# Kernel optimization log

Hardware: AMD Instinct MI355X
Metric: run time of the kernel (lower is better)

The kernel has to match this reference:

```python
import jax, jax.numpy as jnp
import numpy as np

B, D, H = 4096, 256, 1024
TRACE_STEPS = 10
T_FINAL = 1.0


def setup_inputs() -> dict:
    key = jax.random.key(0)
    k0, k1, k2 = jax.random.split(key, 3)
    s1 = 1.0 / np.sqrt(D + 1)
    s2 = 1.0 / np.sqrt(H)
    return {
        "x": jax.random.normal(k0, (B, D), dtype=jnp.float32),
        "W1": jax.random.uniform(k1, (D + 1, H), jnp.float32, -s1, s1),
        "b1": jnp.zeros((H,), jnp.float32),
        "W2": jax.random.uniform(k2, (H, D), jnp.float32, -s2, s2),
        "b2": jnp.zeros((D,), jnp.float32),
    }


def _odefun(params, t, z):
    # FFJORD vector field: tanh MLP on [z, t]. z: [B, D] -> [B, D]
    W1, b1, W2, b2 = params
    tcol = jnp.full((z.shape[0], 1), t, dtype=z.dtype)
    h = jnp.tanh(jnp.concatenate([z, tcol], axis=-1) @ W1 + b1)
    return h @ W2 + b2


def _rademacher(key, shape, dtype):
    # randint(0,2)*2-1, matching the torch probe construction
    return jax.random.randint(key, shape, 0, 2).astype(dtype) * 2.0 - 1.0


def _aug_dynamics(params, t, state, e):
    # state: [B, D+1] = [z | logp]; e: [TRACE_STEPS, B, D] Rademacher probes.
    # torch computes etf = grad((f*e).sum(), z) = e^T J, div = (e^T J)*e summed.
    # e^T J e == e . (J e), so forward-mode jvp gives identical math.
    z = state[:, :-1]
    f = lambda zz: _odefun(params, t, zz)

    def probe(ei):
        f_z, Je = jax.jvp(f, (z,), (ei,))
        return f_z, jnp.sum(Je * ei, axis=-1)  # [B]

    f_z, divs = jax.vmap(probe)(e)
    f_z = f_z[0]                       # primal identical across probes
    div_est = jnp.mean(divs, axis=0)   # average of trace_steps estimates
    return jnp.concatenate([f_z, -div_est[:, None]], axis=-1)


def reference(x, W1, b1, W2, b2):
    params = (W1, b1, W2, b2)
    Bx = x.shape[0]
    ekey = jax.random.key(42)
    probes = lambda i: _rademacher(jax.random.fold_in(ekey, i), (TRACE_STEPS, Bx, D), x.dtype)

    # initial augmented state: [z, logp=0]
    y0 = jnp.concatenate([x, jnp.zeros((Bx, 1), x.dtype)], axis=-1)

    # t_grid = [0, T] with 2 points -> fixed-grid rk4 takes ONE RK4 step of size T
    h = T_FINAL
    g = lambda t, y, i: _aug_dynamics(params, t, y, probes(i))
    k1 = g(0.0, y0, 0)
    k2 = g(0.5 * h, y0 + 0.5 * h * k1, 1)
    k3 = g(0.5 * h, y0 + 0.5 * h * k2, 2)
    k4 = g(h, y0 + h * k3, 3)
    y1 = y0 + (h / 6.0) * (k1 + 2.0 * k2 + 2.0 * k3 + k4)

    # module returns the full trajectory `output`: [len(t_grid), B, D+1]
    return jnp.stack([y0, y1], axis=0)
```

## Files before the change

### kernel.cpp

```cpp
#include <hip/hip_runtime.h>
#include <stdint.h>

#define BATCH 4096
#define DIMD  256
#define DIMH  1024
#define EPAD  264

typedef __attribute__((ext_vector_type(8))) short short8;
typedef __attribute__((ext_vector_type(4))) float float4v;

__host__ __device__ static inline uint32_t rotl32(uint32_t v, int r) {
    return (v << r) | (v >> (32 - r));
}

__host__ __device__ static inline void tf2x32(uint32_t k0, uint32_t k1,
                                              uint32_t c0, uint32_t c1,
                                              uint32_t& o0, uint32_t& o1) {
    uint32_t ks0 = k0, ks1 = k1, ks2 = k0 ^ k1 ^ 0x1BD11BDAu;
    uint32_t x0 = c0 + ks0, x1 = c1 + ks1;
#define TF_R4(a, b, c, d)                                   \
    x0 += x1; x1 = rotl32(x1, a); x1 ^= x0;                 \
    x0 += x1; x1 = rotl32(x1, b); x1 ^= x0;                 \
    x0 += x1; x1 = rotl32(x1, c); x1 ^= x0;                 \
    x0 += x1; x1 = rotl32(x1, d); x1 ^= x0;
    TF_R4(13, 15, 26, 6)  x0 += ks1; x1 += ks2 + 1u;
    TF_R4(17, 29, 16, 24) x0 += ks2; x1 += ks0 + 2u;
    TF_R4(13, 15, 26, 6)  x0 += ks0; x1 += ks1 + 3u;
    TF_R4(17, 29, 16, 24) x0 += ks1; x1 += ks2 + 4u;
    TF_R4(13, 15, 26, 6)  x0 += ks2; x1 += ks0 + 5u;
#undef TF_R4
    o0 = x0; o1 = x1;
}

__device__ static inline short f2bf(float f) {
    uint32_t u = __float_as_uint(f);
    uint32_t r = (u + 0x7FFFu + ((u >> 16) & 1u)) >> 16;
    return (short)r;
}
__device__ static inline float bf2f(short s) {
    return __uint_as_float(((uint32_t)(uint16_t)s) << 16);
}

__global__ __launch_bounds__(256) void k_w1t_bf16(
    const float* __restrict__ W1, short* __restrict__ W1T)
{
    __shared__ float tile[32][33];
    const int bx = blockIdx.x;
    const int by = blockIdx.y;
    const int tx = threadIdx.x, ty = threadIdx.y;
#pragma unroll
    for (int i = 0; i < 4; ++i)
        tile[ty + i * 8][tx] = W1[(by * 32 + ty + i * 8) * DIMH + bx * 32 + tx];
    __syncthreads();
#pragma unroll
    for (int i = 0; i < 4; ++i)
        W1T[(bx * 32 + ty + i * 8) * DIMD + by * 32 + tx] = f2bf(tile[tx][ty + i * 8]);
}

__global__ __launch_bounds__(256) void k_w2t_bf16(
    const float* __restrict__ W2, short* __restrict__ W2T)
{
    __shared__ float tile[32][33];
    const int bx = blockIdx.x;
    const int by = blockIdx.y;
    const int tx = threadIdx.x, ty = threadIdx.y;
#pragma unroll
    for (int i = 0; i < 4; ++i)
        tile[ty + i * 8][tx] = W2[(bx * 32 + ty + i * 8) * DIMD + by * 32 + tx];
    __syncthreads();
#pragma unroll
    for (int i = 0; i < 4; ++i)
        W2T[(by * 32 + ty + i * 8) * DIMH + bx * 32 + tx] = f2bf(tile[tx][ty + i * 8]);
}

__global__ __launch_bounds__(256) void k_w2b_bf16(
    const float* __restrict__ W2, short* __restrict__ W2B)
{
    int idx = blockIdx.x * 256 + threadIdx.x;
    if (idx < DIMH * DIMD) W2B[idx] = f2bf(W2[idx]);
}
__global__ __launch_bounds__(256) void k_zb0(
    const float* __restrict__ x, short* __restrict__ zb)
{
    int idx = blockIdx.x * 256 + threadIdx.x;
    if (idx < BATCH * DIMD) zb[idx] = f2bf(x[idx]);
}

__global__ __launch_bounds__(256) void k_egen(
    uint64_t* __restrict__ Ep, uint32_t key0, uint32_t key1)
{
    const uint32_t j = blockIdx.x * 256 + threadIdx.x;
    uint32_t y0, y1;
    tf2x32(key0, key1, 0u, j, y0, y1);
    uint64_t mask = __ballot(((y0 ^ y1) & 1u) != 0u);
    if ((threadIdx.x & 63) == 0)
        Ep[j >> 6] = mask;
}

__global__ __launch_bounds__(256) void k_pre(
    const short* __restrict__ Zb, const short* __restrict__ W1T,
    const float* __restrict__ W1, const float* __restrict__ b1, float tval,
    short* __restrict__ h_bf)
{
    const int t = threadIdx.x;
    const int wave = t >> 6, lane = t & 63;
    const int col = lane & 15, kq = lane >> 4;
    const int m0 = blockIdx.x * 64 + wave * 16;
    const int n0 = blockIdx.y * 128;

    short8 af[8];
#pragma unroll
    for (int ks = 0; ks < 8; ++ks)
        af[ks] = *(const short8*)&Zb[(m0 + col) * DIMD + ks * 32 + kq * 8];

    float4v acc[8];
#pragma unroll
    for (int ns = 0; ns < 8; ++ns) acc[ns] = (float4v){0.f, 0.f, 0.f, 0.f};

#pragma unroll
    for (int ns = 0; ns < 8; ++ns) {
        const int n = n0 + ns * 16 + col;
        const short* bp = &W1T[n * DIMD + kq * 8];
#pragma unroll
        for (int ks = 0; ks < 8; ++ks) {
            short8 bf = *(const short8*)&bp[ks * 32];
            acc[ns] = __builtin_amdgcn_mfma_f32_16x16x32_bf16(af[ks], bf, acc[ns], 0, 0, 0);
        }
    }
#pragma unroll
    for (int ns = 0; ns < 8; ++ns) {
        const int n = n0 + ns * 16 + col;
        const float add = tval * W1[DIMD * DIMH + n] + b1[n];
#pragma unroll
        for (int r = 0; r < 4; ++r) {
            const int m = m0 + kq * 4 + r;
            h_bf[m * DIMH + n] = f2bf(tanhf(acc[ns][r] + add));
        }
    }
}

__global__ __launch_bounds__(256) void k_fz2(
    const short* __restrict__ Hb, const short* __restrict__ W2T,
    const float* __restrict__ b2, const float* __restrict__ x,
    float* __restrict__ fz, float cnext, int write_zb, short* __restrict__ zb)
{
    const int t = threadIdx.x;
    const int wave = t >> 6, lane = t & 63;
    const int col = lane & 15, kq = lane >> 4;
    const int m0 = blockIdx.x * 16;
    const int n0 = wave * 64;

    float4v acc[4];
#pragma unroll
    for (int ns = 0; ns < 4; ++ns) acc[ns] = (float4v){0.f, 0.f, 0.f, 0.f};

    const short* ap = &Hb[(m0 + col) * DIMH + kq * 8];
    short8 a_cur = *(const short8*)ap;
    short8 b_cur[4];
#pragma unroll
    for (int ns = 0; ns < 4; ++ns)
        b_cur[ns] = *(const short8*)&W2T[(n0 + ns * 16 + col) * DIMH + kq * 8];

    for (int ks = 0; ks < 31; ++ks) {
        short8 a_nxt = *(const short8*)&ap[(ks + 1) * 32];
        short8 b_nxt[4];
#pragma unroll
        for (int ns = 0; ns < 4; ++ns)
            b_nxt[ns] = *(const short8*)&W2T[(n0 + ns * 16 + col) * DIMH + (ks + 1) * 32 + kq * 8];
#pragma unroll
        for (int ns = 0; ns < 4; ++ns)
            acc[ns] = __builtin_amdgcn_mfma_f32_16x16x32_bf16(a_cur, b_cur[ns], acc[ns], 0, 0, 0);
        a_cur = a_nxt;
#pragma unroll
        for (int ns = 0; ns < 4; ++ns) b_cur[ns] = b_nxt[ns];
    }
#pragma unroll
    for (int ns = 0; ns < 4; ++ns)
        acc[ns] = __builtin_amdgcn_mfma_f32_16x16x32_bf16(a_cur, b_cur[ns], acc[ns], 0, 0, 0);

#pragma unroll
    for (int ns = 0; ns < 4; ++ns) {
        const int n = n0 + ns * 16 + col;
        const float bias = b2[n];
#pragma unroll
        for (int r = 0; r < 4; ++r) {
            const int m = m0 + kq * 4 + r;
            const float val = acc[ns][r] + bias;
            fz[m * DIMD + n] = val;
            if (write_zb)
                zb[m * DIMD + n] = f2bf(x[m * DIMD + n] + cnext * val);
        }
    }
}

__global__ __launch_bounds__(256) void k_div2(
    const short* __restrict__ W1T, const short* __restrict__ W2B,
    const short* __restrict__ Hb, const uint64_t* __restrict__ Ep,
    float* __restrict__ divacc)
{
    __shared__ short E[64 * EPAD];
    const int t = threadIdx.x;
    const int nt = blockIdx.x;
    const int b0 = blockIdx.y * 64;
    const int wave = t >> 6, lane = t & 63;
    const int col = lane & 15, kq = lane >> 4;
    const int n = nt * 64 + wave * 16 + col;

    short8 bufr[8], bvfr[8];
#pragma unroll
    for (int ks = 0; ks < 8; ++ks) {
        bufr[ks] = *(const short8*)&W1T[n * DIMD + ks * 32 + kq * 8];
        bvfr[ks] = *(const short8*)&W2B[n * DIMD + ks * 32 + kq * 8];
    }

    float sreg[4][4];
#pragma unroll
    for (int ms = 0; ms < 4; ++ms)
#pragma unroll
        for (int r = 0; r < 4; ++r) {
            float hv = bf2f(Hb[(b0 + ms * 16 + kq * 4 + r) * DIMH + n]);
            sreg[ms][r] = 1.0f - hv * hv;
        }

    float rowacc[4][4];
#pragma unroll
    for (int a = 0; a < 4; ++a)
#pragma unroll
        for (int r = 0; r < 4; ++r) rowacc[a][r] = 0.0f;

    const int erow = t >> 2, ecol = (t & 3) * 64;
    short* const edst = &E[erow * EPAD + ecol];

#pragma unroll 1
    for (int probe = 0; probe < 10; ++probe) {
        __syncthreads();
        uint64_t w = Ep[(size_t)(probe * BATCH + b0) * 4 + t];
#pragma unroll
        for (int i = 0; i < 8; ++i) {
            short8 val;
#pragma unroll
            for (int k = 0; k < 8; ++k)
                val[k] = ((w >> (i * 8 + k)) & 1ull) ? (short)0x3F80 : (short)0xBF80u;
            *(short8*)&edst[i * 8] = val;
        }
        __syncthreads();

#pragma unroll
        for (int ms = 0; ms < 4; ++ms) {
            const short* arow = &E[(ms * 16 + col) * EPAD + kq * 8];
            float4v u = {0.f, 0.f, 0.f, 0.f}, v = {0.f, 0.f, 0.f, 0.f};
#pragma unroll
            for (int ks = 0; ks < 8; ++ks) {
                short8 af = *(const short8*)&arow[ks * 32];
                u = __builtin_amdgcn_mfma_f32_16x16x32_bf16(af, bufr[ks], u, 0, 0, 0);
                v = __builtin_amdgcn_mfma_f32_16x16x32_bf16(af, bvfr[ks], v, 0, 0, 0);
            }
#pragma unroll
            for (int r = 0; r < 4; ++r)
                rowacc[ms][r] += u[r] * sreg[ms][r] * v[r];
        }
    }

#pragma unroll
    for (int ms = 0; ms < 4; ++ms) {
#pragma unroll
        for (int r = 0; r < 4; ++r) {
            float p = rowacc[ms][r];
            p += __shfl_xor(p, 1, 64);
            p += __shfl_xor(p, 2, 64);
            p += __shfl_xor(p, 4, 64);
            p += __shfl_xor(p, 8, 64);
            rowacc[ms][r] = p;
        }
    }
    if (col == 0) {
#pragma unroll
        for (int ms = 0; ms < 4; ++ms)
#pragma unroll
            for (int r = 0; r < 4; ++r)
                atomicAdd(&divacc[b0 + ms * 16 + kq * 4 + r], rowacc[ms][r] * 0.1f);
    }
}

__global__ __launch_bounds__(256) void k_out(
    const float* __restrict__ x, const float* __restrict__ fz,
    const float* __restrict__ divacc, float* __restrict__ out)
{
    const int idx = blockIdx.x * 256 + threadIdx.x;
    const int TOT = BATCH * (DIMD + 1);
    if (idx >= TOT) return;
    const int b = idx / (DIMD + 1);
    const int c = idx - b * (DIMD + 1);
    const float sixth = 1.0f / 6.0f;
    if (c < DIMD) {
        float xv = x[b * DIMD + c];
        int o = b * DIMD + c;
        float f1 = fz[o];
        float f2 = fz[BATCH * DIMD + o];
        float f3 = fz[2 * BATCH * DIMD + o];
        float f4 = fz[3 * BATCH * DIMD + o];
        out[idx] = xv;
        out[TOT + idx] = xv + (f1 + 2.0f * f2 + 2.0f * f3 + f4) * sixth;
    } else {
        float d1 = divacc[b];
        float d2 = divacc[BATCH + b];
        float d3 = divacc[2 * BATCH + b];
        float d4 = divacc[3 * BATCH + b];
        out[idx] = 0.0f;
        out[TOT + idx] = -(d1 + 2.0f * d2 + 2.0f * d3 + d4) * sixth;
    }
}

extern "C" void kernel_launch(void* const* d_in, const int* in_sizes, int n_in,
                              void* d_out, int out_size, void* d_ws, size_t ws_size,
                              hipStream_t stream) {
    const float* x  = (const float*)d_in[0];
    const float* W1 = (const float*)d_in[1];
    const float* b1 = (const float*)d_in[2];
    const float* W2 = (const float*)d_in[3];
    const float* b2 = (const float*)d_in[4];
    float* out = (float*)d_out;

    char* ws = (char*)d_ws;
    short* hb   = (short*)(ws);
    float* fz   = (float*)(ws + 8388608);
    short* zb   = (short*)(ws + 25165824);
    short* w1t  = (short*)(ws + 27262976);
    short* w2b  = (short*)(ws + 27787264);
    short* w2t  = (short*)(ws + 28311552);
    float* dv   = (float*)(ws + 28835840);
    uint64_t* ep = (uint64_t*)(ws + 28901376);

    uint32_t keys[4][2];
    for (uint32_t i = 0; i < 4; ++i) {
        uint32_t f0, f1, g0, g1;
        tf2x32(0u, 42u, 0u, i, f0, f1);
        tf2x32(f0, f1, 0u, 1u, g0, g1);
        keys[i][0] = g0;
        keys[i][1] = g1;
    }

    hipMemsetAsync(dv, 0, 4 * BATCH * sizeof(float), stream);

    k_w1t_bf16<<<dim3(32, 8), dim3(32, 8), 0, stream>>>(W1, w1t);
    k_w2t_bf16<<<dim3(32, 8), dim3(32, 8), 0, stream>>>(W2, w2t);
    k_w2b_bf16<<<(DIMH * DIMD + 255) / 256, 256, 0, stream>>>(W2, w2b);
    k_zb0<<<(BATCH * DIMD + 255) / 256, 256, 0, stream>>>(x, zb);

    const float tvals[4] = {0.0f, 0.5f, 0.5f, 1.0f};
    const float cnext[4] = {0.5f, 0.5f, 1.0f, 0.0f};
    const int NEL = 10 * BATCH * DIMD;
    for (int s = 0; s < 4; ++s) {
        k_egen<<<NEL / 256, 256, 0, stream>>>(ep, keys[s][0], keys[s][1]);
        k_pre<<<dim3(64, 8), 256, 0, stream>>>(zb, w1t, W1, b1, tvals[s], hb);
        k_div2<<<dim3(16, 64), 256, 0, stream>>>(w1t, w2b, hb, ep,
                                                 dv + (size_t)s * BATCH);
        k_fz2<<<256, 256, 0, stream>>>(hb, w2t, b2, x,
                                       fz + (size_t)s * BATCH * DIMD,
                                       cnext[s], (s < 3) ? 1 : 0, zb);
    }
    int tot = BATCH * (DIMD + 1);
    k_out<<<(tot + 255) / 256, 256, 0, stream>>>(x, fz, dv, out);
}
```

Measured before the change: 592.4 us.

## Fuse hidden-layer GEMM into divergence kernel and batch probe generation upfront

Merges the first-layer GEMM plus tanh into the divergence kernel, so each block computes its own h tile and derivative in registers instead of reading h back from global memory. The four weight and input conversion kernels and the memset are folded into one prep kernel, and probe bits for all four RK stages are generated in a single launch. The E-tile load indexing is also changed to match. This removes several launches and one pass over h per stage. The cost is extra register pressure in the fused kernel and uncoalesced transposed reads in the prep kernel.

```diff
diff --git a/kernel.cpp b/kernel.cpp
--- a/kernel.cpp
+++ b/kernel.cpp
@@ -5,9 +5,12 @@
 #define DIMD  256
 #define DIMH  1024
 #define EPAD  264
+#define NEPW  163840
 
 typedef __attribute__((ext_vector_type(8))) short short8;
 typedef __attribute__((ext_vector_type(4))) float float4v;
+
+struct Keys4 { uint32_t a[4]; uint32_t b[4]; };
 
 __host__ __device__ static inline uint32_t rotl32(uint32_t v, int r) {
     return (v << r) | (v >> (32 - r));
@@ -37,165 +40,49 @@
     uint32_t r = (u + 0x7FFFu + ((u >> 16) & 1u)) >> 16;
     return (short)r;
 }
-__device__ static inline float bf2f(short s) {
-    return __uint_as_float(((uint32_t)(uint16_t)s) << 16);
-}
-
-__global__ __launch_bounds__(256) void k_w1t_bf16(
-    const float* __restrict__ W1, short* __restrict__ W1T)
-{
-    __shared__ float tile[32][33];
-    const int bx = blockIdx.x;
-    const int by = blockIdx.y;
-    const int tx = threadIdx.x, ty = threadIdx.y;
-#pragma unroll
-    for (int i = 0; i < 4; ++i)
-        tile[ty + i * 8][tx] = W1[(by * 32 + ty + i * 8) * DIMH + bx * 32 + tx];
-    __syncthreads();
-#pragma unroll
-    for (int i = 0; i < 4; ++i)
-        W1T[(bx * 32 + ty + i * 8) * DIMD + by * 32 + tx] = f2bf(tile[tx][ty + i * 8]);
-}
-
-__global__ __launch_bounds__(256) void k_w2t_bf16(
-    const float* __restrict__ W2, short* __restrict__ W2T)
-{
-    __shared__ float tile[32][33];
-    const int bx = blockIdx.x;
-    const int by = blockIdx.y;
-    const int tx = threadIdx.x, ty = threadIdx.y;
-#pragma unroll
-    for (int i = 0; i < 4; ++i)
-        tile[ty + i * 8][tx] = W2[(bx * 32 + ty + i * 8) * DIMD + by * 32 + tx];
-    __syncthreads();
-#pragma unroll
-    for (int i = 0; i < 4; ++i)
-        W2T[(by * 32 + ty + i * 8) * DIMH + bx * 32 + tx] = f2bf(tile[tx][ty + i * 8]);
-}
-
-__global__ __launch_bounds__(256) void k_w2b_bf16(
-    const float* __restrict__ W2, short* __restrict__ W2B)
-{
-    int idx = blockIdx.x * 256 + threadIdx.x;
-    if (idx < DIMH * DIMD) W2B[idx] = f2bf(W2[idx]);
-}
-__global__ __launch_bounds__(256) void k_zb0(
-    const float* __restrict__ x, short* __restrict__ zb)
-{
-    int idx = blockIdx.x * 256 + threadIdx.x;
-    if (idx < BATCH * DIMD) zb[idx] = f2bf(x[idx]);
-}
-
-__global__ __launch_bounds__(256) void k_egen(
-    uint64_t* __restrict__ Ep, uint32_t key0, uint32_t key1)
-{
+
+__global__ __launch_bounds__(256) void k_prep(
+    const float* __restrict__ x,  const float* __restrict__ W1,
+    const float* __restrict__ W2, short* __restrict__ W1T,
+    short* __restrict__ W2B, short* __restrict__ W2T,
+    short* __restrict__ zb, float* __restrict__ dv)
+{
+    const int idx = blockIdx.x * 256 + threadIdx.x;
+    if (idx < 262144) {
+        const int n = idx >> 8, d = idx & 255;
+        W1T[idx] = f2bf(W1[d * DIMH + n]);
+    } else if (idx < 524288) {
+        const int i = idx - 262144;
+        W2B[i] = f2bf(W2[i]);
+    } else if (idx < 786432) {
+        const int i = idx - 524288;
+        const int d = i >> 10, k = i & 1023;
+        W2T[i] = f2bf(W2[k * DIMD + d]);
+    } else if (idx < 1835008) {
+        const int i = idx - 786432;
+        zb[i] = f2bf(x[i]);
+    } else if (idx < 1851392) {
+        dv[idx - 1835008] = 0.0f;
+    }
+}
+
+__global__ __launch_bounds__(256) void k_egen4(
+    uint64_t* __restrict__ Ep, Keys4 keys)
+{
+    const int s = blockIdx.y;
     const uint32_t j = blockIdx.x * 256 + threadIdx.x;
     uint32_t y0, y1;
-    tf2x32(key0, key1, 0u, j, y0, y1);
+    tf2x32(keys.a[s], keys.b[s], 0u, j, y0, y1);
     uint64_t mask = __ballot(((y0 ^ y1) & 1u) != 0u);
     if ((threadIdx.x & 63) == 0)
-        Ep[j >> 6] = mask;
-}
-
-__global__ __launch_bounds__(256) void k_pre(
+        Ep[(size_t)s * NEPW + (j >> 6)] = mask;
+}
+
+__global__ __launch_bounds__(256) void k_pre_div(
     const short* __restrict__ Zb, const short* __restrict__ W1T,
-    const float* __restrict__ W1, const float* __restrict__ b1, float tval,
-    short* __restrict__ h_bf)
-{
-    const int t = threadIdx.x;
-    const int wave = t >> 6, lane = t & 63;
-    const int col = lane & 15, kq = lane >> 4;
-    const int m0 = blockIdx.x * 64 + wave * 16;
-    const int n0 = blockIdx.y * 128;
-
-    short8 af[8];
-#pragma unroll
-    for (int ks = 0; ks < 8; ++ks)
-        af[ks] = *(const short8*)&Zb[(m0 + col) * DIMD + ks * 32 + kq * 8];
-
-    float4v acc[8];
-#pragma unroll
-    for (int ns = 0; ns < 8; ++ns) acc[ns] = (float4v){0.f, 0.f, 0.f, 0.f};
-
-#pragma unroll
-    for (int ns = 0; ns < 8; ++ns) {
-        const int n = n0 + ns * 16 + col;
-        const short* bp = &W1T[n * DIMD + kq * 8];
-#pragma unroll
-        for (int ks = 0; ks < 8; ++ks) {
-            short8 bf = *(const short8*)&bp[ks * 32];
-            acc[ns] = __builtin_amdgcn_mfma_f32_16x16x32_bf16(af[ks], bf, acc[ns], 0, 0, 0);
-        }
-    }
-#pragma unroll
-    for (int ns = 0; ns < 8; ++ns) {
-        const int n = n0 + ns * 16 + col;
-        const float add = tval * W1[DIMD * DIMH + n] + b1[n];
-#pragma unroll
-        for (int r = 0; r < 4; ++r) {
-            const int m = m0 + kq * 4 + r;
-            h_bf[m * DIMH + n] = f2bf(tanhf(acc[ns][r] + add));
-        }
-    }
-}
-
-__global__ __launch_bounds__(256) void k_fz2(
-    const short* __restrict__ Hb, const short* __restrict__ W2T,
-    const float* __restrict__ b2, const float* __restrict__ x,
-    float* __restrict__ fz, float cnext, int write_zb, short* __restrict__ zb)
-{
-    const int t = threadIdx.x;
-    const int wave = t >> 6, lane = t & 63;
-    const int col = lane & 15, kq = lane >> 4;
-    const int m0 = blockIdx.x * 16;
-    const int n0 = wave * 64;
-
-    float4v acc[4];
-#pragma unroll
-    for (int ns = 0; ns < 4; ++ns) acc[ns] = (float4v){0.f, 0.f, 0.f, 0.f};
-
-    const short* ap = &Hb[(m0 + col) * DIMH + kq * 8];
-    short8 a_cur = *(const short8*)ap;
-    short8 b_cur[4];
-#pragma unroll
-    for (int ns = 0; ns < 4; ++ns)
-        b_cur[ns] = *(const short8*)&W2T[(n0 + ns * 16 + col) * DIMH + kq * 8];
-
-    for (int ks = 0; ks < 31; ++ks) {
-        short8 a_nxt = *(const short8*)&ap[(ks + 1) * 32];
-        short8 b_nxt[4];
-#pragma unroll
-        for (int ns = 0; ns < 4; ++ns)
-            b_nxt[ns] = *(const short8*)&W2T[(n0 + ns * 16 + col) * DIMH + (ks + 1) * 32 + kq * 8];
-#pragma unroll
-        for (int ns = 0; ns < 4; ++ns)
-            acc[ns] = __builtin_amdgcn_mfma_f32_16x16x32_bf16(a_cur, b_cur[ns], acc[ns], 0, 0, 0);
-        a_cur = a_nxt;
-#pragma unroll
-        for (int ns = 0; ns < 4; ++ns) b_cur[ns] = b_nxt[ns];
-    }
-#pragma unroll
-    for (int ns = 0; ns < 4; ++ns)
-        acc[ns] = __builtin_amdgcn_mfma_f32_16x16x32_bf16(a_cur, b_cur[ns], acc[ns], 0, 0, 0);
-
-#pragma unroll
-    for (int ns = 0; ns < 4; ++ns) {
-        const int n = n0 + ns * 16 + col;
-        const float bias = b2[n];
-#pragma unroll
-        for (int r = 0; r < 4; ++r) {
-            const int m = m0 + kq * 4 + r;
-            const float val = acc[ns][r] + bias;
-            fz[m * DIMD + n] = val;
-            if (write_zb)
-                zb[m * DIMD + n] = f2bf(x[m * DIMD + n] + cnext * val);
-        }
-    }
-}
-
-__global__ __launch_bounds__(256) void k_div2(
-    const short* __restrict__ W1T, const short* __restrict__ W2B,
-    const short* __restrict__ Hb, const uint64_t* __restrict__ Ep,
+    const short* __restrict__ W2B, const float* __restrict__ W1,
+    const float* __restrict__ b1, float tval,
+    const uint64_t* __restrict__ Ep, short* __restrict__ h_bf,
     float* __restrict__ divacc)
 {
     __shared__ short E[64 * EPAD];
@@ -206,21 +93,33 @@
     const int col = lane & 15, kq = lane >> 4;
     const int n = nt * 64 + wave * 16 + col;
 
-    short8 bufr[8], bvfr[8];
-#pragma unroll
-    for (int ks = 0; ks < 8; ++ks) {
+    short8 bufr[8];
+#pragma unroll
+    for (int ks = 0; ks < 8; ++ks)
         bufr[ks] = *(const short8*)&W1T[n * DIMD + ks * 32 + kq * 8];
+
+    float sreg[4][4];
+    const float add = tval * W1[DIMD * DIMH + n] + b1[n];
+#pragma unroll
+    for (int ms = 0; ms < 4; ++ms) {
+        float4v acc = {0.f, 0.f, 0.f, 0.f};
+#pragma unroll
+        for (int ks = 0; ks < 8; ++ks) {
+            short8 af = *(const short8*)&Zb[(b0 + ms * 16 + col) * DIMD + ks * 32 + kq * 8];
+            acc = __builtin_amdgcn_mfma_f32_16x16x32_bf16(af, bufr[ks], acc, 0, 0, 0);
+        }
+#pragma unroll
+        for (int r = 0; r < 4; ++r) {
+            float hv = tanhf(acc[r] + add);
+            h_bf[(b0 + ms * 16 + kq * 4 + r) * DIMH + n] = f2bf(hv);
+            sreg[ms][r] = 1.0f - hv * hv;
+        }
+    }
+
+    short8 bvfr[8];
+#pragma unroll
+    for (int ks = 0; ks < 8; ++ks)
         bvfr[ks] = *(const short8*)&W2B[n * DIMD + ks * 32 + kq * 8];
-    }
-
-    float sreg[4][4];
-#pragma unroll
-    for (int ms = 0; ms < 4; ++ms)
-#pragma unroll
-        for (int r = 0; r < 4; ++r) {
-            float hv = bf2f(Hb[(b0 + ms * 16 + kq * 4 + r) * DIMH + n]);
-            sreg[ms][r] = 1.0f - hv * hv;
-        }
 
     float rowacc[4][4];
 #pragma unroll
@@ -228,13 +127,14 @@
 #pragma unroll
         for (int r = 0; r < 4; ++r) rowacc[a][r] = 0.0f;
 
-    const int erow = t >> 2, ecol = (t & 3) * 64;
-    short* const edst = &E[erow * EPAD + ecol];
+    const int erow = t & 63, ecg = t >> 6;
+    short* const edst = &E[erow * EPAD + ecg * 64];
+    const uint64_t* const esrc = Ep + (size_t)b0 * 4 + erow * 4 + ecg;
 
 #pragma unroll 1
     for (int probe = 0; probe < 10; ++probe) {
         __syncthreads();
-        uint64_t w = Ep[(size_t)(probe * BATCH + b0) * 4 + t];
+        uint64_t w = esrc[(size_t)probe * BATCH * 4];
 #pragma unroll
         for (int i = 0; i < 8; ++i) {
             short8 val;
@@ -279,6 +179,60 @@
 #pragma unroll
             for (int r = 0; r < 4; ++r)
                 atomicAdd(&divacc[b0 + ms * 16 + kq * 4 + r], rowacc[ms][r] * 0.1f);
+    }
+}
+
+__global__ __launch_bounds__(256) void k_fz2(
+    const short* __restrict__ Hb, const short* __restrict__ W2T,
+    const float* __restrict__ b2, const float* __restrict__ x,
+    float* __restrict__ fz, float cnext, int write_zb, short* __restrict__ zb)
+{
+    const int t = threadIdx.x;
+    const int wave = t >> 6, lane = t & 63;
+    const int col = lane & 15, kq = lane >> 4;
+    const int m0 = blockIdx.x * 16;
+    const int n0 = wave * 64;
+
+    float4v acc[4];
+#pragma unroll
+    for (int ns = 0; ns < 4; ++ns) acc[ns] = (float4v){0.f, 0.f, 0.f, 0.f};
+
+    const short* ap = &Hb[(m0 + col) * DIMH + kq * 8];
+    short8 a_cur = *(const short8*)ap;
+    short8 b_cur[4];
+#pragma unroll
+    for (int ns = 0; ns < 4; ++ns)
+        b_cur[ns] = *(const short8*)&W2T[(n0 + ns * 16 + col) * DIMH + kq * 8];
+
+    for (int ks = 0; ks < 31; ++ks) {
+        short8 a_nxt = *(const short8*)&ap[(ks + 1) * 32];
+        short8 b_nxt[4];
+#pragma unroll
+        for (int ns = 0; ns < 4; ++ns)
+            b_nxt[ns] = *(const short8*)&W2T[(n0 + ns * 16 + col) * DIMH + (ks + 1) * 32 + kq * 8];
+#pragma unroll
+        for (int ns = 0; ns < 4; ++ns)
+            acc[ns] = __builtin_amdgcn_mfma_f32_16x16x32_bf16(a_cur, b_cur[ns], acc[ns], 0, 0, 0);
+        a_cur = a_nxt;
+#pragma unroll
+        for (int ns = 0; ns < 4; ++ns) b_cur[ns] = b_nxt[ns];
+    }
+#pragma unroll
+    for (int ns = 0; ns < 4; ++ns)
+        acc[ns] = __builtin_amdgcn_mfma_f32_16x16x32_bf16(a_cur, b_cur[ns], acc[ns], 0, 0, 0);
+
+#pragma unroll
+    for (int ns = 0; ns < 4; ++ns) {
+        const int n = n0 + ns * 16 + col;
+        const float bias = b2[n];
+#pragma unroll
+        for (int r = 0; r < 4; ++r) {
+            const int m = m0 + kq * 4 + r;
+            const float val = acc[ns][r] + bias;
+            fz[m * DIMD + n] = val;
+            if (write_zb)
+                zb[m * DIMD + n] = f2bf(x[m * DIMD + n] + cnext * val);
+        }
     }
 }
 
@@ -322,39 +276,33 @@
     float* out = (float*)d_out;
 
     char* ws = (char*)d_ws;
-    short* hb   = (short*)(ws);
-    float* fz   = (float*)(ws + 8388608);
-    short* zb   = (short*)(ws + 25165824);
-    short* w1t  = (short*)(ws + 27262976);
-    short* w2b  = (short*)(ws + 27787264);
-    short* w2t  = (short*)(ws + 28311552);
-    float* dv   = (float*)(ws + 28835840);
+    short* hb    = (short*)(ws);
+    float* fz    = (float*)(ws + 8388608);
+    short* zb    = (short*)(ws + 25165824);
+    short* w1t   = (short*)(ws + 27262976);
+    short* w2b   = (short*)(ws + 27787264);
+    short* w2t   = (short*)(ws + 28311552);
+    float* dv    = (float*)(ws + 28835840);
     uint64_t* ep = (uint64_t*)(ws + 28901376);
 
-    uint32_t keys[4][2];
+    Keys4 keys;
     for (uint32_t i = 0; i < 4; ++i) {
         uint32_t f0, f1, g0, g1;
         tf2x32(0u, 42u, 0u, i, f0, f1);
         tf2x32(f0, f1, 0u, 1u, g0, g1);
-        keys[i][0] = g0;
-        keys[i][1] = g1;
-    }
-
-    hipMemsetAsync(dv, 0, 4 * BATCH * sizeof(float), stream);
-
-    k_w1t_bf16<<<dim3(32, 8), dim3(32, 8), 0, stream>>>(W1, w1t);
-    k_w2t_bf16<<<dim3(32, 8), dim3(32, 8), 0, stream>>>(W2, w2t);
-    k_w2b_bf16<<<(DIMH * DIMD + 255) / 256, 256, 0, stream>>>(W2, w2b);
-    k_zb0<<<(BATCH * DIMD + 255) / 256, 256, 0, stream>>>(x, zb);
+        keys.a[i] = g0;
+        keys.b[i] = g1;
+    }
+
+    k_prep<<<7232, 256, 0, stream>>>(x, W1, W2, w1t, w2b, w2t, zb, dv);
+    k_egen4<<<dim3(40960, 4), 256, 0, stream>>>(ep, keys);
 
     const float tvals[4] = {0.0f, 0.5f, 0.5f, 1.0f};
     const float cnext[4] = {0.5f, 0.5f, 1.0f, 0.0f};
-    const int NEL = 10 * BATCH * DIMD;
     for (int s = 0; s < 4; ++s) {
-        k_egen<<<NEL / 256, 256, 0, stream>>>(ep, keys[s][0], keys[s][1]);
-        k_pre<<<dim3(64, 8), 256, 0, stream>>>(zb, w1t, W1, b1, tvals[s], hb);
-        k_div2<<<dim3(16, 64), 256, 0, stream>>>(w1t, w2b, hb, ep,
-                                                 dv + (size_t)s * BATCH);
+        k_pre_div<<<dim3(16, 64), 256, 0, stream>>>(
+            zb, w1t, w2b, W1, b1, tvals[s], ep + (size_t)s * NEPW,
+            hb, dv + (size_t)s * BATCH);
         k_fz2<<<256, 256, 0, stream>>>(hb, w2t, b2, x,
                                        fz + (size_t)s * BATCH * DIMD,
                                        cnext[s], (s < 3) ? 1 : 0, zb);
```

Result: faster. 523.9 us (-11.6%).
